# Performance work log

Hardware: AMD Instinct MI355X
Metric: run time of the kernel (lower is better)

Reference implementation:

```python
import jax, jax.numpy as jnp
import numpy as np

B, S, E = 2, 2048, 2048
H, HKV = 16, 4
G = H // HKV
QLR, KVLR = 1024, 512
DN, DR, DV = 128, 64, 128
DQK = DN + DR
EPS = 1.1920929e-07  # torch.finfo(float32).eps, F.rms_norm default


def rms_norm(x):
    return x * jax.lax.rsqrt(jnp.mean(x * x, axis=-1, keepdims=True) + EPS)


def apply_rope(x, cos, sin):
    # x: [B, S, h, D]; pairs are adjacent elements (torch view_as_complex convention)
    x0, x1 = x[..., 0::2], x[..., 1::2]            # [B,S,h,D/2]
    c = cos[None, :, None, :]
    s = sin[None, :, None, :]
    r0 = x0 * c - x1 * s
    r1 = x0 * s + x1 * c
    return jnp.stack([r0, r1], axis=-1).reshape(x.shape)


def setup_inputs() -> dict:
    key = jax.random.key(0)
    ks = jax.random.split(key, 8)
    inv_freq = 1.0 / (10000.0 ** (np.arange(0, DR, 2, dtype=np.float32) / DR))  # [DR/2]
    ang = np.arange(S, dtype=np.float32)[:, None] * inv_freq[None, :]           # [S, DR/2]
    return {
        "x": jax.random.normal(ks[0], (B, S, E), jnp.float32),
        "freqs_cos": jnp.asarray(np.cos(ang), jnp.float32),
        "freqs_sin": jnp.asarray(np.sin(ang), jnp.float32),
        "Wqa": jax.random.normal(ks[1], (QLR, E), jnp.float32) * (E ** -0.5),
        "Wqb": jax.random.normal(ks[2], (H * DQK, QLR), jnp.float32) * (QLR ** -0.5),
        "Wkva": jax.random.normal(ks[3], (KVLR + DR, E), jnp.float32) * (E ** -0.5),
        "Wkvb": jax.random.normal(ks[4], (HKV * (DN + DV), KVLR), jnp.float32) * (KVLR ** -0.5),
        "Wo": jax.random.normal(ks[5], (E, H * DV), jnp.float32) * ((H * DV) ** -0.5),
    }


def reference(x, freqs_cos, freqs_sin, Wqa, Wqb, Wkva, Wkvb, Wo):
    # Q path: low-rank down-proj -> rmsnorm -> up-proj
    q = rms_norm(x @ Wqa.T) @ Wqb.T                       # [B,S,H*DQK]
    q = q.reshape(B, S, H, DQK)
    q_nope, q_rope = q[..., :DN], q[..., DN:]
    q_rope = apply_rope(q_rope, freqs_cos, freqs_sin)
    q = jnp.concatenate([q_nope, q_rope], axis=-1)        # [B,S,H,DQK]

    # KV path: joint down-proj, shared rope key, up-proj of latent
    kv_a = x @ Wkva.T                                     # [B,S,KVLR+DR]
    kv_latent, k_rope = kv_a[..., :KVLR], kv_a[..., KVLR:]
    k_rope = jnp.broadcast_to(k_rope[:, :, None, :], (B, S, HKV, DR))
    k_rope = apply_rope(k_rope, freqs_cos, freqs_sin)     # [B,S,HKV,DR]
    kv = (rms_norm(kv_latent) @ Wkvb.T).reshape(B, S, HKV, DN + DV)
    k_nope, v = kv[..., :DN], kv[..., DN:]
    k = jnp.concatenate([k_nope, k_rope], axis=-1)        # [B,S,HKV,DQK]

    # GQA causal SDPA: group G query heads per kv head
    qg = q.reshape(B, S, HKV, G, DQK)
    scores = jnp.einsum("bsngd,btnd->bngst", qg, k) * (DQK ** -0.5)  # [B,HKV,G,S,S]
    causal = jnp.tril(jnp.ones((S, S), bool))
    scores = jnp.where(causal, scores, jnp.finfo(scores.dtype).min)
    attn = jax.nn.softmax(scores, axis=-1)
    o = jnp.einsum("bngst,btnd->bsngd", attn, v).reshape(B, S, H * DV)
    return o @ Wo.T                                        # [B,S,E]
```

## Files before the change

kernel.cpp:

```cpp
#include <hip/hip_runtime.h>
#include <cstdint>
#include <cstddef>

typedef __attribute__((ext_vector_type(4))) float f32x4;
typedef __attribute__((ext_vector_type(2))) float f32x2;
typedef __attribute__((ext_vector_type(8))) short short8;
typedef __attribute__((ext_vector_type(8))) __bf16 bf16x8;
typedef unsigned short u16;
typedef unsigned int u32;
typedef __attribute__((ext_vector_type(2))) unsigned int u32x2;
typedef __attribute__((ext_vector_type(4))) unsigned short u16x4;
typedef __attribute__((ext_vector_type(2))) unsigned short u16x2;

#define EPS_RMS 1.1920929e-07f

__device__ __forceinline__ u16 f2bf(float f) {
  union { float f; unsigned u; } v; v.f = f;
  unsigned r = v.u + 0x7FFFu + ((v.u >> 16) & 1u);
  return (u16)(r >> 16);
}
__device__ __forceinline__ float b2f(u16 x) {
  union { unsigned u; float f; } v; v.u = ((unsigned)x) << 16;
  return v.f;
}
__device__ __forceinline__ u32 cvt_pk_bf16(float lo, float hi) {
  u32 r;
  asm("v_cvt_pk_bf16_f32 %0, %1, %2" : "=v"(r) : "v"(lo), "v"(hi));
  return r;
}

template <typename V>
__device__ __forceinline__ auto mfma_try(V a, V b, f32x4 c, int)
    -> decltype(__builtin_amdgcn_mfma_f32_16x16x32_bf16(a, b, c, 0, 0, 0)) {
  return __builtin_amdgcn_mfma_f32_16x16x32_bf16(a, b, c, 0, 0, 0);
}
template <typename V>
__device__ __forceinline__ f32x4 mfma_try(V a, V b, f32x4 c, long) {
  return __builtin_amdgcn_mfma_f32_16x16x32_bf16(
      __builtin_bit_cast(bf16x8, a), __builtin_bit_cast(bf16x8, b), c, 0, 0, 0);
}
__device__ __forceinline__ f32x4 mfma_bf16(short8 a, short8 b, f32x4 c) {
  return mfma_try(a, b, c, 0);
}

__device__ __forceinline__ void load_lds16(u16* lds, const u16* g) {
  auto* gp = reinterpret_cast<const __attribute__((address_space(1))) unsigned int*>(
      reinterpret_cast<uintptr_t>(g));
  auto* lp = reinterpret_cast<__attribute__((address_space(3))) unsigned int*>(
      reinterpret_cast<uintptr_t>(lds));
  __builtin_amdgcn_global_load_lds(gp, lp, 16, 0, 0);
}

__device__ __forceinline__ float fast_exp2(float x) {
  return __builtin_amdgcn_exp2f(x);
}

template <int CTRL>
__device__ __forceinline__ float dpp_step(float v) {
  int t = __builtin_amdgcn_update_dpp(0, __builtin_bit_cast(int, v), CTRL, 0xF, 0xF, true);
  return __builtin_bit_cast(float, t);
}

__global__ __launch_bounds__(256) void cvt_bf16(const float* __restrict__ in,
                                                u16* __restrict__ out, int n4) {
  int i = blockIdx.x * 256 + threadIdx.x;
  if (i >= n4) return;
  f32x4 v = ((const f32x4*)in)[i];
  u16x4 o = {f2bf(v.x), f2bf(v.y), f2bf(v.z), f2bf(v.w)};
  ((u16x4*)out)[i] = o;
}

__global__ __launch_bounds__(256) void build_wacat(const float* __restrict__ Wqa,
                                                   const float* __restrict__ Wkva,
                                                   u16* __restrict__ out) {
  int i = blockIdx.x * 256 + threadIdx.x;
  if (i >= 851968) return;
  int r = i >> 9;
  int c4 = i & 511;
  f32x4 v = {0.f, 0.f, 0.f, 0.f};
  if (r < 1024) v = ((const f32x4*)Wqa)[r * 512 + c4];
  else if (r < 1600) v = ((const f32x4*)Wkva)[(r - 1024) * 512 + c4];
  u16x4 o = {f2bf(v.x), f2bf(v.y), f2bf(v.z), f2bf(v.w)};
  ((u16x4*)out)[i] = o;
}

template <typename OutT, int EPI>
__global__ __launch_bounds__(256) void gemm_bt(const u16* __restrict__ A,
                                               const u16* __restrict__ B,
                                               OutT* __restrict__ C,
                                               int M, int N, int K, int gx,
                                               const float* __restrict__ fc,
                                               const float* __restrict__ fs,
                                               u16* __restrict__ aux) {
  __shared__ __align__(16) u16 As[2][128 * 64];
  __shared__ __align__(16) u16 Bs[2][128 * 64];
  const int nwg = gridDim.x;
  const int cpx = nwg >> 3;
  const int swz = (blockIdx.x & 7) * cpx + (blockIdx.x >> 3);
  const int by = swz / gx, bxx = swz - by * gx;
  const int tid = threadIdx.x;
  const int lane = tid & 63, w = tid >> 6;
  const int wr = w >> 1, wc = w & 1;
  const int l16 = lane & 15, lg = lane >> 4;
  const int row0 = by * 128, col0 = bxx * 128;

  const u16* Ab = A + (size_t)row0 * K;
  const u16* Bb = B + (size_t)col0 * K;

  f32x4 acc[4][4] = {};

  int soff[4], ldst[4];
#pragma unroll
  for (int j = 0; j < 4; ++j) {
    int c = j * 256 + tid;
    int row = c >> 3;
    int rb = (c & 7) << 4;
    int sb = rb ^ ((row & 7) << 4);
    soff[j] = row * K + (sb >> 1);
    ldst[j] = c * 8;
  }

#pragma unroll
  for (int j = 0; j < 4; ++j) load_lds16(As[0] + ldst[j], Ab + soff[j]);
#pragma unroll
  for (int j = 0; j < 4; ++j) load_lds16(Bs[0] + ldst[j], Bb + soff[j]);
  __syncthreads();

  int cur = 0;
  for (int k0 = 0; k0 < K; k0 += 64) {
    if (k0 + 64 < K) {
#pragma unroll
      for (int j = 0; j < 4; ++j) load_lds16(As[cur ^ 1] + ldst[j], Ab + soff[j] + k0 + 64);
#pragma unroll
      for (int j = 0; j < 4; ++j) load_lds16(Bs[cur ^ 1] + ldst[j], Bb + soff[j] + k0 + 64);
    }
    const u16* Ac = As[cur];
    const u16* Bc = Bs[cur];
    short8 a[2][4], bfr[2][4];
#pragma unroll
    for (int mt = 0; mt < 4; ++mt) {
      const int rowA = wr * 64 + mt * 16 + l16;
      const int sw = (rowA & 7) << 4;
#pragma unroll
      for (int kk = 0; kk < 2; ++kk)
        a[kk][mt] = *(const short8*)(Ac + rowA * 64 + (((kk * 64 + lg * 16) ^ sw) >> 1));
    }
#pragma unroll
    for (int nt = 0; nt < 4; ++nt) {
      const int rowB = wc * 64 + nt * 16 + l16;
      const int sw = (rowB & 7) << 4;
#pragma unroll
      for (int kk = 0; kk < 2; ++kk)
        bfr[kk][nt] = *(const short8*)(Bc + rowB * 64 + (((kk * 64 + lg * 16) ^ sw) >> 1));
    }
#pragma unroll
    for (int kk = 0; kk < 2; ++kk)
#pragma unroll
      for (int mt = 0; mt < 4; ++mt)
#pragma unroll
        for (int nt = 0; nt < 4; ++nt)
          acc[mt][nt] = mfma_bf16(a[kk][mt], bfr[kk][nt], acc[mt][nt]);
    __syncthreads();
    cur ^= 1;
  }

  if constexpr (EPI == 0 || EPI == 1) {
#pragma unroll
    for (int mt = 0; mt < 4; ++mt)
#pragma unroll
      for (int nt = 0; nt < 4; ++nt)
#pragma unroll
        for (int i = 0; i < 4; ++i) {
          int row = row0 + wr * 64 + mt * 16 + lg * 4 + i;
          int col = col0 + wc * 64 + nt * 16 + l16;
          if constexpr (EPI == 0)
            C[(size_t)row * N + col] = acc[mt][nt][i];
          else
            C[(size_t)row * N + col] = f2bf(acc[mt][nt][i]);
        }
  } else if constexpr (EPI == 2) {
    const float qscale = 0.07216878364870322f * 1.4426950408889634f;
#pragma unroll
    for (int mt = 0; mt < 4; ++mt)
#pragma unroll
      for (int nt = 0; nt < 4; ++nt) {
        int col = col0 + wc * 64 + nt * 16 + l16;
        int hh = ((col >> 6) * 43) >> 7;
        int cin = col - hh * 192;
        int m = (cin - 128) >> 1;
#pragma unroll
        for (int i = 0; i < 4; ++i) {
          int row = row0 + wr * 64 + mt * 16 + lg * 4 + i;
          int bb = row >> 11, ss = row & 2047;
          float v = acc[mt][nt][i];
          float pv = dpp_step<0xB1>(v);
          float val = v;
          if (cin >= 128) {
            float c = fc[ss * 32 + m], sn = fs[ss * 32 + m];
            val = ((l16 & 1) == 0) ? (v * c - pv * sn) : (pv * sn + v * c);
          }
          ((u16*)C)[((size_t)((bb * 16 + hh) * 2048 + ss)) * 192 + cin] = f2bf(val * qscale);
        }
      }
  } else {
#pragma unroll
    for (int mt = 0; mt < 4; ++mt)
#pragma unroll
      for (int nt = 0; nt < 4; ++nt) {
        int col = col0 + wc * 64 + nt * 16 + l16;
        int nn = col >> 8, cin = col & 255;
        int rowb = row0 + wr * 64 + mt * 16 + lg * 4;
        int bb = rowb >> 11, ss0 = rowb & 2047;
        if (cin < 128) {
#pragma unroll
          for (int i = 0; i < 4; ++i)
            ((u16*)C)[((size_t)((bb * 4 + nn) * 2048 + ss0 + i)) * 192 + cin] =
                f2bf(acc[mt][nt][i]);
        } else {
          int dv = cin - 128;
          u16x4 o = {f2bf(acc[mt][nt][0]), f2bf(acc[mt][nt][1]),
                     f2bf(acc[mt][nt][2]), f2bf(acc[mt][nt][3])};
          *(u16x4*)(aux + ((size_t)((bb * 4 + nn) * 128 + dv)) * 2048 + ss0) = o;
        }
      }
  }
}

__global__ __launch_bounds__(256) void rms_fused(const u16* __restrict__ c1b,
                                                 const float* __restrict__ fc,
                                                 const float* __restrict__ fs,
                                                 u16* __restrict__ qlat,
                                                 u16* __restrict__ kvlat,
                                                 u16* __restrict__ Ka) {
  __shared__ float smq[4], smk[4];
  int t = blockIdx.x;
  const u16* row = c1b + (size_t)t * 1664;
  u16x4 v4u = ((const u16x4*)row)[threadIdx.x];
  u16x2 v2u = ((const u16x2*)(row + 1024))[threadIdx.x];
  float v4x = b2f(v4u.x), v4y = b2f(v4u.y), v4z = b2f(v4u.z), v4w = b2f(v4u.w);
  float v2x = b2f(v2u.x), v2y = b2f(v2u.y);
  float sq = v4x * v4x + v4y * v4y + v4z * v4z + v4w * v4w;
  float sk = v2x * v2x + v2y * v2y;
#pragma unroll
  for (int off = 32; off; off >>= 1) { sq += __shfl_xor(sq, off); sk += __shfl_xor(sk, off); }
  if ((threadIdx.x & 63) == 0) { smq[threadIdx.x >> 6] = sq; smk[threadIdx.x >> 6] = sk; }
  __syncthreads();
  float rq = rsqrtf((smq[0] + smq[1] + smq[2] + smq[3]) * (1.0f / 1024.0f) + EPS_RMS);
  float rk = rsqrtf((smk[0] + smk[1] + smk[2] + smk[3]) * (1.0f / 512.0f) + EPS_RMS);
  u16x4 oq = {f2bf(v4x * rq), f2bf(v4y * rq), f2bf(v4z * rq), f2bf(v4w * rq)};
  ((u16x4*)(qlat + (size_t)t * 1024))[threadIdx.x] = oq;
  u16x2 ok = {f2bf(v2x * rk), f2bf(v2y * rk)};
  ((u16x2*)(kvlat + (size_t)t * 512))[threadIdx.x] = ok;
  if (threadIdx.x < 32) {
    int bb = t >> 11, s = t & 2047;
    int m = threadIdx.x;
    float x0 = b2f(row[1536 + 2 * m]), x1 = b2f(row[1537 + 2 * m]);
    float c = fc[s * 32 + m], sn = fs[s * 32 + m];
    u16 r0 = f2bf(x0 * c - x1 * sn);
    u16 r1 = f2bf(x0 * sn + x1 * c);
#pragma unroll
    for (int nn = 0; nn < 4; ++nn) {
      size_t base = ((size_t)((bb * 4 + nn) * 2048 + s)) * 192 + 128;
      Ka[base + 2 * m] = r0;
      Ka[base + 2 * m + 1] = r1;
    }
  }
}

__global__ __launch_bounds__(256, 2) void attn_kernel(const u16* __restrict__ Qa,
                                                      const u16* __restrict__ Ka,
                                                      const u16* __restrict__ VTp,
                                                      u16* __restrict__ Ob) {
  __shared__ __align__(16) u16 Ks[64 * 192];
  __shared__ __align__(16) u16 Vs[128 * 64];
  __shared__ __align__(16) u32 Ppk[4][32][36];
  const int gid = blockIdx.x;
  const int bx = (gid < 256) ? (15 - (gid >> 5)) : ((gid - 256) >> 5);
  const int hb = gid & 31;
  const int b = hb >> 4;
  const int h = hb & 15;
  const int n = h >> 2;
  const int tid = threadIdx.x;
  const int lane = tid & 63;
  const int w = tid >> 6;
  const int l16 = lane & 15;
  const int lg = lane >> 4;

  const u16* Qp = Qa + ((size_t)((b * 16 + h) * 2048 + bx * 128 + w * 32)) * 192;
  const u16* Kp = Ka + ((size_t)((b * 4 + n) * 2048)) * 192;
  const u16* Vp = VTp + ((size_t)((b * 4 + n) * 128)) * 2048;

  int oK[6];
#pragma unroll
  for (int j = 0; j < 6; ++j) {
    int c = j * 256 + tid;
    int row = (c * 2731) >> 16;
    int rb = (c - row * 24) << 4;
    int sb = rb ^ ((row & 7) << 4);
    oK[j] = row * 192 + (sb >> 1);
  }
  int oV[4];
#pragma unroll
  for (int j = 0; j < 4; ++j) {
    int c = j * 256 + tid;
    int row = c >> 3;
    int rb = (c & 7) << 4;
    int sb = rb ^ ((row & 7) << 4);
    oV[j] = row * 2048 + (sb >> 1);
  }

  short8 qf[2][6];
#pragma unroll
  for (int g = 0; g < 2; ++g)
#pragma unroll
    for (int kc = 0; kc < 6; ++kc)
      qf[g][kc] = *(const short8*)(Qp + (size_t)(g * 16 + l16) * 192 + kc * 32 + lg * 8);

  float mrow[2], lrow[2];
  f32x4 oacc[2][8];
#pragma unroll
  for (int g = 0; g < 2; ++g) { mrow[g] = -1e30f; lrow[g] = 0.f; }
#pragma unroll
  for (int g = 0; g < 2; ++g)
#pragma unroll
    for (int vb = 0; vb < 8; ++vb) oacc[g][vb] = (f32x4){0.f, 0.f, 0.f, 0.f};

  const int wrow = bx * 128 + w * 32;
  const int NT = 2 * bx + 2;

  f32x4 kreg[6], vreg[4];
#pragma unroll
  for (int j = 0; j < 6; ++j) kreg[j] = *(const f32x4*)(Kp + oK[j]);
#pragma unroll
  for (int j = 0; j < 4; ++j) vreg[j] = *(const f32x4*)(Vp + oV[j]);

  for (int kt = 0; kt < NT; ++kt) {
    const int kb = kt * 64;
    __syncthreads();
#pragma unroll
    for (int j = 0; j < 6; ++j) *(f32x4*)(Ks + (j * 256 + tid) * 8) = kreg[j];
#pragma unroll
    for (int j = 0; j < 4; ++j) *(f32x4*)(Vs + (j * 256 + tid) * 8) = vreg[j];
    __syncthreads();
    if (kt + 1 < NT) {
      const int kb2 = kb + 64;
#pragma unroll
      for (int j = 0; j < 6; ++j)
        kreg[j] = *(const f32x4*)(Kp + oK[j] + (size_t)kb2 * 192);
#pragma unroll
      for (int j = 0; j < 4; ++j)
        vreg[j] = *(const f32x4*)(Vp + oV[j] + kb2);
    }
    if (kb > wrow + 31) continue;

    f32x4 sc[2][4];
#pragma unroll
    for (int g = 0; g < 2; ++g)
#pragma unroll
      for (int kn = 0; kn < 4; ++kn) sc[g][kn] = (f32x4){0.f, 0.f, 0.f, 0.f};
    __builtin_amdgcn_s_setprio(1);
#pragma unroll
    for (int kn = 0; kn < 4; ++kn) {
      const int rk = kn * 16 + l16;
      const u16* kbase = Ks + rk * 192;
      const int sw = (rk & 7) << 4;
#pragma unroll
      for (int kc = 0; kc < 6; ++kc) {
        short8 kf = *(const short8*)(kbase + (((kc * 64 + lg * 16) ^ sw) >> 1));
        sc[0][kn] = mfma_bf16(kf, qf[0][kc], sc[0][kn]);
        sc[1][kn] = mfma_bf16(kf, qf[1][kc], sc[1][kn]);
      }
    }
    __builtin_amdgcn_s_setprio(0);
    if (kb + 63 > wrow) {
#pragma unroll
      for (int g = 0; g < 2; ++g) {
        const int qabs = wrow + g * 16 + l16;
#pragma unroll
        for (int kn = 0; kn < 4; ++kn)
#pragma unroll
          for (int i = 0; i < 4; ++i)
            if (kb + kn * 16 + lg * 4 + i > qabs) sc[g][kn][i] = -1e30f;
      }
    }
    float pmax[2];
    int need = 0;
#pragma unroll
    for (int g = 0; g < 2; ++g) {
      float v = -1e30f;
#pragma unroll
      for (int kn = 0; kn < 4; ++kn)
        v = fmaxf(v, fmaxf(fmaxf(sc[g][kn][0], sc[g][kn][1]),
                           fmaxf(sc[g][kn][2], sc[g][kn][3])));
      v = fmaxf(v, __shfl_xor(v, 16));
      v = fmaxf(v, __shfl_xor(v, 32));
      pmax[g] = v;
      need |= (v > mrow[g] + 8.0f) ? 1 : 0;
    }
    if (__any(need)) {
#pragma unroll
      for (int g = 0; g < 2; ++g) {
        float mn = fmaxf(mrow[g], pmax[g]);
        float al = fast_exp2(mrow[g] - mn);
        mrow[g] = mn;
        lrow[g] *= al;
#pragma unroll
        for (int i = 0; i < 4; ++i) {
          float alq = __shfl(al, lg * 4 + i);
#pragma unroll
          for (int vb = 0; vb < 8; ++vb) oacc[g][vb][i] *= alq;
        }
      }
    }
#pragma unroll
    for (int g = 0; g < 2; ++g) {
      float rs = 0.f;
#pragma unroll
      for (int kn = 0; kn < 4; ++kn)
#pragma unroll
        for (int i = 0; i < 4; ++i) {
          float p = fast_exp2(sc[g][kn][i] - mrow[g]);
          sc[g][kn][i] = p;
          rs += p;
        }
      rs += __shfl_xor(rs, 16);
      rs += __shfl_xor(rs, 32);
      lrow[g] += rs;
    }
#pragma unroll
    for (int g = 0; g < 2; ++g) {
      const int r = g * 16 + l16;
#pragma unroll
      for (int kn = 0; kn < 4; ++kn) {
        u32x2 pk = {cvt_pk_bf16(sc[g][kn][0], sc[g][kn][1]),
                    cvt_pk_bf16(sc[g][kn][2], sc[g][kn][3])};
        *(u32x2*)&Ppk[w][r][kn * 8 + 2 * lg] = pk;
      }
    }
    short8 pa[2][2];
#pragma unroll
    for (int g = 0; g < 2; ++g) {
      const int r = g * 16 + l16;
      pa[g][0] = *(const short8*)&Ppk[w][r][lg * 4];
      pa[g][1] = *(const short8*)&Ppk[w][r][16 + lg * 4];
    }
    __builtin_amdgcn_s_setprio(1);
#pragma unroll
    for (int vb = 0; vb < 8; ++vb) {
      const int rv = vb * 16 + l16;
      const u16* vbase = Vs + rv * 64;
      const int swv = (rv & 7) << 4;
      short8 v0 = *(const short8*)(vbase + (((lg * 16) ^ swv) >> 1));
      short8 v1 = *(const short8*)(vbase + (((64 + lg * 16) ^ swv) >> 1));
      oacc[0][vb] = mfma_bf16(pa[0][0], v0, oacc[0][vb]);
      oacc[1][vb] = mfma_bf16(pa[1][0], v0, oacc[1][vb]);
      oacc[0][vb] = mfma_bf16(pa[0][1], v1, oacc[0][vb]);
      oacc[1][vb] = mfma_bf16(pa[1][1], v1, oacc[1][vb]);
    }
    __builtin_amdgcn_s_setprio(0);
  }
#pragma unroll
  for (int g = 0; g < 2; ++g) {
    float inv = 1.0f / lrow[g];
#pragma unroll
    for (int i = 0; i < 4; ++i) {
      float invq = __shfl(inv, lg * 4 + i);
      int srow = wrow + g * 16 + lg * 4 + i;
      size_t base = ((size_t)(b * 2048 + srow)) * 2048 + h * 128;
#pragma unroll
      for (int vb = 0; vb < 8; ++vb)
        Ob[base + vb * 16 + l16] = f2bf(oacc[g][vb][i] * invq);
    }
  }
}

extern "C" void kernel_launch(void* const* d_in, const int* in_sizes, int n_in,
                              void* d_out, int out_size, void* d_ws, size_t ws_size,
                              hipStream_t stream) {
  const float* x = (const float*)d_in[0];
  const float* fc = (const float*)d_in[1];
  const float* fs = (const float*)d_in[2];
  const float* Wqa = (const float*)d_in[3];
  const float* Wqb = (const float*)d_in[4];
  const float* Wkva = (const float*)d_in[5];
  const float* Wkvb = (const float*)d_in[6];
  const float* Wo = (const float*)d_in[7];
  float* out = (float*)d_out;

  char* ws = (char*)d_ws;
  u16* xb    = (u16*)(ws + 0);
  u16* wacat = (u16*)(ws + 16777216);
  u16* wqb   = (u16*)(ws + 23592960);
  u16* wkvb  = (u16*)(ws + 29884416);
  u16* wo    = (u16*)(ws + 30932992);
  u16* c1b   = (u16*)(ws + 39321600);
  u16* qlat  = (u16*)(ws + 52953088);
  u16* kvlat = (u16*)(ws + 61341696);
  u16* obf   = (u16*)(ws + 65536000);
  u16* qattn = (u16*)(ws + 82313216);
  u16* kattn = (u16*)(ws + 107479040);
  u16* vt    = (u16*)(ws + 113770496);
  if (ws_size < 117964800u) return;

  cvt_bf16<<<8192, 256, 0, stream>>>(x, xb, 2097152);
  build_wacat<<<3328, 256, 0, stream>>>(Wqa, Wkva, wacat);
  cvt_bf16<<<3072, 256, 0, stream>>>(Wqb, wqb, 786432);
  cvt_bf16<<<512, 256, 0, stream>>>(Wkvb, wkvb, 131072);
  cvt_bf16<<<4096, 256, 0, stream>>>(Wo, wo, 1048576);

  gemm_bt<u16, 1><<<416, 256, 0, stream>>>(xb, wacat, c1b, 4096, 1664, 2048, 13,
                                           nullptr, nullptr, nullptr);
  rms_fused<<<4096, 256, 0, stream>>>(c1b, fc, fs, qlat, kvlat, kattn);
  gemm_bt<u16, 2><<<768, 256, 0, stream>>>(qlat, wqb, qattn, 4096, 3072, 1024, 24,
                                           fc, fs, nullptr);
  gemm_bt<u16, 3><<<256, 256, 0, stream>>>(kvlat, wkvb, kattn, 4096, 1024, 512, 8,
                                           nullptr, nullptr, vt);
  attn_kernel<<<512, 256, 0, stream>>>(qattn, kattn, vt, obf);
  gemm_bt<float, 0><<<512, 256, 0, stream>>>(obf, wo, out, 4096, 2048, 2048, 16,
                                             nullptr, nullptr, nullptr);
}
```

Measured before the change: 244.7 us.

## Widen GEMM tiles to 128x256 with 8 waves and deeper LDS prefetch pipeline

Replaces the 128x128, 4-wave GEMM with a 128x256 tile using 512 threads (2x4 waves). It prefetches two K-tiles ahead, splits each K-step into two MFMA phases, and uses explicit waitcnt, sched and s_barrier control plus setprio around the MFMA bursts, aiming to hide global-to-LDS latency and improve reuse of the A tile. The concatenated weight is padded to 1792 rows so that N divides the wider tile, which adds some wasted compute. The workspace is also re-laid out with qattn aliasing xb. The larger LDS footprint and fewer blocks may lower occupancy or leave CUs idle on small GEMMs.

```diff
diff --git a/kernel.cpp b/kernel.cpp
--- a/kernel.cpp
+++ b/kernel.cpp
@@ -74,7 +74,7 @@
                                                    const float* __restrict__ Wkva,
                                                    u16* __restrict__ out) {
   int i = blockIdx.x * 256 + threadIdx.x;
-  if (i >= 851968) return;
+  if (i >= 917504) return;
   int r = i >> 9;
   int c4 = i & 511;
   f32x4 v = {0.f, 0.f, 0.f, 0.f};
@@ -85,82 +85,124 @@
 }
 
 template <typename OutT, int EPI>
-__global__ __launch_bounds__(256) void gemm_bt(const u16* __restrict__ A,
-                                               const u16* __restrict__ B,
-                                               OutT* __restrict__ C,
-                                               int M, int N, int K, int gx,
-                                               const float* __restrict__ fc,
-                                               const float* __restrict__ fs,
-                                               u16* __restrict__ aux) {
+__global__ __launch_bounds__(512, 2) void gemm_bt2(const u16* __restrict__ A,
+                                                   const u16* __restrict__ B,
+                                                   OutT* __restrict__ C,
+                                                   int M, int N, int K, int gx,
+                                                   const float* __restrict__ fc,
+                                                   const float* __restrict__ fs,
+                                                   u16* __restrict__ aux) {
   __shared__ __align__(16) u16 As[2][128 * 64];
-  __shared__ __align__(16) u16 Bs[2][128 * 64];
+  __shared__ __align__(16) u16 Bs[2][256 * 64];
   const int nwg = gridDim.x;
   const int cpx = nwg >> 3;
   const int swz = (blockIdx.x & 7) * cpx + (blockIdx.x >> 3);
   const int by = swz / gx, bxx = swz - by * gx;
   const int tid = threadIdx.x;
   const int lane = tid & 63, w = tid >> 6;
-  const int wr = w >> 1, wc = w & 1;
+  const int wr = w >> 2, wc = w & 3;
   const int l16 = lane & 15, lg = lane >> 4;
-  const int row0 = by * 128, col0 = bxx * 128;
+  const int row0 = by * 128, col0 = bxx * 256;
 
   const u16* Ab = A + (size_t)row0 * K;
   const u16* Bb = B + (size_t)col0 * K;
 
   f32x4 acc[4][4] = {};
 
-  int soff[4], ldst[4];
+  int soffA[2], ldA[2], soffB[4], ldB[4];
+#pragma unroll
+  for (int j = 0; j < 2; ++j) {
+    int c = j * 512 + tid;
+    int row = c >> 3;
+    int sb = ((c & 7) << 4) ^ ((row & 7) << 4);
+    soffA[j] = row * K + (sb >> 1);
+    ldA[j] = c * 8;
+  }
 #pragma unroll
   for (int j = 0; j < 4; ++j) {
-    int c = j * 256 + tid;
+    int c = j * 512 + tid;
     int row = c >> 3;
-    int rb = (c & 7) << 4;
-    int sb = rb ^ ((row & 7) << 4);
-    soff[j] = row * K + (sb >> 1);
-    ldst[j] = c * 8;
-  }
-
-#pragma unroll
-  for (int j = 0; j < 4; ++j) load_lds16(As[0] + ldst[j], Ab + soff[j]);
-#pragma unroll
-  for (int j = 0; j < 4; ++j) load_lds16(Bs[0] + ldst[j], Bb + soff[j]);
-  __syncthreads();
+    int sb = ((c & 7) << 4) ^ ((row & 7) << 4);
+    soffB[j] = row * K + (sb >> 1);
+    ldB[j] = c * 8;
+  }
+
+  const int nT = K >> 6;
+
+#pragma unroll
+  for (int j = 0; j < 2; ++j) load_lds16(As[0] + ldA[j], Ab + soffA[j]);
+#pragma unroll
+  for (int j = 0; j < 4; ++j) load_lds16(Bs[0] + ldB[j], Bb + soffB[j]);
+#pragma unroll
+  for (int j = 0; j < 2; ++j) load_lds16(As[1] + ldA[j], Ab + soffA[j] + 64);
+#pragma unroll
+  for (int j = 0; j < 4; ++j) load_lds16(Bs[1] + ldB[j], Bb + soffB[j] + 64);
+  asm volatile("s_waitcnt vmcnt(6)" ::: "memory");
+  __builtin_amdgcn_sched_barrier(0);
+  __builtin_amdgcn_s_barrier();
 
   int cur = 0;
-  for (int k0 = 0; k0 < K; k0 += 64) {
-    if (k0 + 64 < K) {
-#pragma unroll
-      for (int j = 0; j < 4; ++j) load_lds16(As[cur ^ 1] + ldst[j], Ab + soff[j] + k0 + 64);
-#pragma unroll
-      for (int j = 0; j < 4; ++j) load_lds16(Bs[cur ^ 1] + ldst[j], Bb + soff[j] + k0 + 64);
-    }
+  for (int t = 0; t < nT; ++t) {
     const u16* Ac = As[cur];
     const u16* Bc = Bs[cur];
-    short8 a[2][4], bfr[2][4];
+    short8 a0[4], b0[4];
 #pragma unroll
     for (int mt = 0; mt < 4; ++mt) {
-      const int rowA = wr * 64 + mt * 16 + l16;
-      const int sw = (rowA & 7) << 4;
-#pragma unroll
-      for (int kk = 0; kk < 2; ++kk)
-        a[kk][mt] = *(const short8*)(Ac + rowA * 64 + (((kk * 64 + lg * 16) ^ sw) >> 1));
+      int r = wr * 64 + mt * 16 + l16;
+      a0[mt] = *(const short8*)(Ac + r * 64 + (((lg * 16) ^ ((r & 7) << 4)) >> 1));
     }
 #pragma unroll
     for (int nt = 0; nt < 4; ++nt) {
-      const int rowB = wc * 64 + nt * 16 + l16;
-      const int sw = (rowB & 7) << 4;
-#pragma unroll
-      for (int kk = 0; kk < 2; ++kk)
-        bfr[kk][nt] = *(const short8*)(Bc + rowB * 64 + (((kk * 64 + lg * 16) ^ sw) >> 1));
-    }
-#pragma unroll
-    for (int kk = 0; kk < 2; ++kk)
-#pragma unroll
-      for (int mt = 0; mt < 4; ++mt)
-#pragma unroll
-        for (int nt = 0; nt < 4; ++nt)
-          acc[mt][nt] = mfma_bf16(a[kk][mt], bfr[kk][nt], acc[mt][nt]);
-    __syncthreads();
+      int r = wc * 64 + nt * 16 + l16;
+      b0[nt] = *(const short8*)(Bc + r * 64 + (((lg * 16) ^ ((r & 7) << 4)) >> 1));
+    }
+    __builtin_amdgcn_s_barrier();
+    asm volatile("s_waitcnt lgkmcnt(0)" ::: "memory");
+    __builtin_amdgcn_sched_barrier(0);
+    __builtin_amdgcn_s_setprio(1);
+#pragma unroll
+    for (int mt = 0; mt < 4; ++mt)
+#pragma unroll
+      for (int nt = 0; nt < 4; ++nt)
+        acc[mt][nt] = mfma_bf16(a0[mt], b0[nt], acc[mt][nt]);
+    __builtin_amdgcn_s_setprio(0);
+    short8 a1[4], b1[4];
+#pragma unroll
+    for (int mt = 0; mt < 4; ++mt) {
+      int r = wr * 64 + mt * 16 + l16;
+      a1[mt] = *(const short8*)(Ac + r * 64 + (((64 + lg * 16) ^ ((r & 7) << 4)) >> 1));
+    }
+#pragma unroll
+    for (int nt = 0; nt < 4; ++nt) {
+      int r = wc * 64 + nt * 16 + l16;
+      b1[nt] = *(const short8*)(Bc + r * 64 + (((64 + lg * 16) ^ ((r & 7) << 4)) >> 1));
+    }
+    asm volatile("s_waitcnt lgkmcnt(0)" ::: "memory");
+    __builtin_amdgcn_sched_barrier(0);
+    __builtin_amdgcn_s_barrier();
+    if (t + 2 < nT) {
+      const int ko = (t + 2) << 6;
+#pragma unroll
+      for (int j = 0; j < 2; ++j) load_lds16(As[cur] + ldA[j], Ab + soffA[j] + ko);
+#pragma unroll
+      for (int j = 0; j < 4; ++j) load_lds16(Bs[cur] + ldB[j], Bb + soffB[j] + ko);
+    }
+    __builtin_amdgcn_s_setprio(1);
+#pragma unroll
+    for (int mt = 0; mt < 4; ++mt)
+#pragma unroll
+      for (int nt = 0; nt < 4; ++nt)
+        acc[mt][nt] = mfma_bf16(a1[mt], b1[nt], acc[mt][nt]);
+    __builtin_amdgcn_s_setprio(0);
+    if (t + 1 < nT) {
+      if (t + 2 < nT) {
+        asm volatile("s_waitcnt vmcnt(6)" ::: "memory");
+      } else {
+        asm volatile("s_waitcnt vmcnt(0)" ::: "memory");
+      }
+      __builtin_amdgcn_sched_barrier(0);
+      __builtin_amdgcn_s_barrier();
+    }
     cur ^= 1;
   }
 
@@ -234,7 +276,7 @@
                                                  u16* __restrict__ Ka) {
   __shared__ float smq[4], smk[4];
   int t = blockIdx.x;
-  const u16* row = c1b + (size_t)t * 1664;
+  const u16* row = c1b + (size_t)t * 1792;
   u16x4 v4u = ((const u16x4*)row)[threadIdx.x];
   u16x2 v2u = ((const u16x2*)(row + 1024))[threadIdx.x];
   float v4x = b2f(v4u.x), v4y = b2f(v4u.y), v4z = b2f(v4u.z), v4w = b2f(v4u.w);
@@ -490,32 +532,32 @@
   char* ws = (char*)d_ws;
   u16* xb    = (u16*)(ws + 0);
   u16* wacat = (u16*)(ws + 16777216);
-  u16* wqb   = (u16*)(ws + 23592960);
-  u16* wkvb  = (u16*)(ws + 29884416);
-  u16* wo    = (u16*)(ws + 30932992);
-  u16* c1b   = (u16*)(ws + 39321600);
-  u16* qlat  = (u16*)(ws + 52953088);
-  u16* kvlat = (u16*)(ws + 61341696);
-  u16* obf   = (u16*)(ws + 65536000);
-  u16* qattn = (u16*)(ws + 82313216);
-  u16* kattn = (u16*)(ws + 107479040);
-  u16* vt    = (u16*)(ws + 113770496);
-  if (ws_size < 117964800u) return;
+  u16* qattn = (u16*)(ws + 0);
+  u16* wqb   = (u16*)(ws + 25165824);
+  u16* wkvb  = (u16*)(ws + 31457280);
+  u16* wo    = (u16*)(ws + 32505856);
+  u16* c1b   = (u16*)(ws + 40894464);
+  u16* qlat  = (u16*)(ws + 55574528);
+  u16* kvlat = (u16*)(ws + 63963136);
+  u16* obf   = (u16*)(ws + 68157440);
+  u16* kattn = (u16*)(ws + 84934656);
+  u16* vt    = (u16*)(ws + 91226112);
+  if (ws_size < 95420416u) return;
 
   cvt_bf16<<<8192, 256, 0, stream>>>(x, xb, 2097152);
-  build_wacat<<<3328, 256, 0, stream>>>(Wqa, Wkva, wacat);
+  build_wacat<<<3584, 256, 0, stream>>>(Wqa, Wkva, wacat);
   cvt_bf16<<<3072, 256, 0, stream>>>(Wqb, wqb, 786432);
   cvt_bf16<<<512, 256, 0, stream>>>(Wkvb, wkvb, 131072);
   cvt_bf16<<<4096, 256, 0, stream>>>(Wo, wo, 1048576);
 
-  gemm_bt<u16, 1><<<416, 256, 0, stream>>>(xb, wacat, c1b, 4096, 1664, 2048, 13,
-                                           nullptr, nullptr, nullptr);
+  gemm_bt2<u16, 1><<<224, 512, 0, stream>>>(xb, wacat, c1b, 4096, 1792, 2048, 7,
+                                            nullptr, nullptr, nullptr);
   rms_fused<<<4096, 256, 0, stream>>>(c1b, fc, fs, qlat, kvlat, kattn);
-  gemm_bt<u16, 2><<<768, 256, 0, stream>>>(qlat, wqb, qattn, 4096, 3072, 1024, 24,
-                                           fc, fs, nullptr);
-  gemm_bt<u16, 3><<<256, 256, 0, stream>>>(kvlat, wkvb, kattn, 4096, 1024, 512, 8,
-                                           nullptr, nullptr, vt);
+  gemm_bt2<u16, 2><<<384, 512, 0, stream>>>(qlat, wqb, qattn, 4096, 3072, 1024, 12,
+                                            fc, fs, nullptr);
+  gemm_bt2<u16, 3><<<128, 512, 0, stream>>>(kvlat, wkvb, kattn, 4096, 1024, 512, 4,
+                                            nullptr, nullptr, vt);
   attn_kernel<<<512, 256, 0, stream>>>(qattn, kattn, vt, obf);
-  gemm_bt<float, 0><<<512, 256, 0, stream>>>(obf, wo, out, 4096, 2048, 2048, 16,
-                                             nullptr, nullptr, nullptr);
-}
+  gemm_bt2<float, 0><<<256, 512, 0, stream>>>(obf, wo, out, 4096, 2048, 2048, 8,
+                                              nullptr, nullptr, nullptr);
+}
```

Result: slower. 253.5 us (+3.6%).

## Shrink attention blocks to 64 query rows and read V directly from global

Applied to the files above, without the earlier changes.

The attention kernel now uses 128-thread blocks, each covering 64 query rows, and launches twice as many blocks. The block-to-tile map uses a serpentine order across bands to balance causal work. V tiles are no longer staged in shared memory; each wave loads V fragments straight from global memory before the PV MFMAs. This cuts LDS use and barrier traffic and raises occupancy, at the cost of redundant global V loads per wave and less K reuse per block.

```diff
diff --git a/kernel.cpp b/kernel.cpp
--- a/kernel.cpp
+++ b/kernel.cpp
@@ -267,18 +267,20 @@
   }
 }
 
-__global__ __launch_bounds__(256, 2) void attn_kernel(const u16* __restrict__ Qa,
+__global__ __launch_bounds__(128, 2) void attn_kernel(const u16* __restrict__ Qa,
                                                       const u16* __restrict__ Ka,
                                                       const u16* __restrict__ VTp,
                                                       u16* __restrict__ Ob) {
   __shared__ __align__(16) u16 Ks[64 * 192];
-  __shared__ __align__(16) u16 Vs[128 * 64];
-  __shared__ __align__(16) u32 Ppk[4][32][36];
+  __shared__ __align__(16) u32 Ppk[2][32][36];
   const int gid = blockIdx.x;
-  const int bx = (gid < 256) ? (15 - (gid >> 5)) : ((gid - 256) >> 5);
-  const int hb = gid & 31;
-  const int b = hb >> 4;
-  const int h = hb & 15;
+  const int band = gid >> 8, idx = gid & 255;
+  const int pos = (band & 1) ? (255 - idx) : idx;
+  const int rank = band * 256 + pos;
+  const int qx = 31 - (rank >> 5);
+  const int bh = rank & 31;
+  const int b = bh >> 4;
+  const int h = bh & 15;
   const int n = h >> 2;
   const int tid = threadIdx.x;
   const int lane = tid & 63;
@@ -286,28 +288,19 @@
   const int l16 = lane & 15;
   const int lg = lane >> 4;
 
-  const u16* Qp = Qa + ((size_t)((b * 16 + h) * 2048 + bx * 128 + w * 32)) * 192;
+  const u16* Qp = Qa + ((size_t)((b * 16 + h) * 2048 + qx * 64 + w * 32)) * 192;
   const u16* Kp = Ka + ((size_t)((b * 4 + n) * 2048)) * 192;
   const u16* Vp = VTp + ((size_t)((b * 4 + n) * 128)) * 2048;
 
-  int oK[6];
-#pragma unroll
-  for (int j = 0; j < 6; ++j) {
-    int c = j * 256 + tid;
+  int oK[12];
+#pragma unroll
+  for (int j = 0; j < 12; ++j) {
+    int c = j * 128 + tid;
     int row = (c * 2731) >> 16;
     int rb = (c - row * 24) << 4;
     int sb = rb ^ ((row & 7) << 4);
     oK[j] = row * 192 + (sb >> 1);
   }
-  int oV[4];
-#pragma unroll
-  for (int j = 0; j < 4; ++j) {
-    int c = j * 256 + tid;
-    int row = c >> 3;
-    int rb = (c & 7) << 4;
-    int sb = rb ^ ((row & 7) << 4);
-    oV[j] = row * 2048 + (sb >> 1);
-  }
 
   short8 qf[2][6];
 #pragma unroll
@@ -325,33 +318,25 @@
 #pragma unroll
     for (int vb = 0; vb < 8; ++vb) oacc[g][vb] = (f32x4){0.f, 0.f, 0.f, 0.f};
 
-  const int wrow = bx * 128 + w * 32;
-  const int NT = 2 * bx + 2;
-
-  f32x4 kreg[6], vreg[4];
-#pragma unroll
-  for (int j = 0; j < 6; ++j) kreg[j] = *(const f32x4*)(Kp + oK[j]);
-#pragma unroll
-  for (int j = 0; j < 4; ++j) vreg[j] = *(const f32x4*)(Vp + oV[j]);
+  const int wrow = qx * 64 + w * 32;
+  const int NT = qx + 1;
+
+  f32x4 kreg[12];
+#pragma unroll
+  for (int j = 0; j < 12; ++j) kreg[j] = *(const f32x4*)(Kp + oK[j]);
 
   for (int kt = 0; kt < NT; ++kt) {
     const int kb = kt * 64;
     __syncthreads();
 #pragma unroll
-    for (int j = 0; j < 6; ++j) *(f32x4*)(Ks + (j * 256 + tid) * 8) = kreg[j];
-#pragma unroll
-    for (int j = 0; j < 4; ++j) *(f32x4*)(Vs + (j * 256 + tid) * 8) = vreg[j];
+    for (int j = 0; j < 12; ++j) *(f32x4*)(Ks + (j * 128 + tid) * 8) = kreg[j];
     __syncthreads();
     if (kt + 1 < NT) {
       const int kb2 = kb + 64;
 #pragma unroll
-      for (int j = 0; j < 6; ++j)
+      for (int j = 0; j < 12; ++j)
         kreg[j] = *(const f32x4*)(Kp + oK[j] + (size_t)kb2 * 192);
-#pragma unroll
-      for (int j = 0; j < 4; ++j)
-        vreg[j] = *(const f32x4*)(Vp + oV[j] + kb2);
-    }
-    if (kb > wrow + 31) continue;
+    }
 
     f32x4 sc[2][4];
 #pragma unroll
@@ -446,16 +431,23 @@
     }
     __builtin_amdgcn_s_setprio(1);
 #pragma unroll
-    for (int vb = 0; vb < 8; ++vb) {
-      const int rv = vb * 16 + l16;
-      const u16* vbase = Vs + rv * 64;
-      const int swv = (rv & 7) << 4;
-      short8 v0 = *(const short8*)(vbase + (((lg * 16) ^ swv) >> 1));
-      short8 v1 = *(const short8*)(vbase + (((64 + lg * 16) ^ swv) >> 1));
-      oacc[0][vb] = mfma_bf16(pa[0][0], v0, oacc[0][vb]);
-      oacc[1][vb] = mfma_bf16(pa[1][0], v0, oacc[1][vb]);
-      oacc[0][vb] = mfma_bf16(pa[0][1], v1, oacc[0][vb]);
-      oacc[1][vb] = mfma_bf16(pa[1][1], v1, oacc[1][vb]);
+    for (int hf = 0; hf < 2; ++hf) {
+      short8 vv[4][2];
+#pragma unroll
+      for (int q = 0; q < 4; ++q) {
+        const int vb = hf * 4 + q;
+        const u16* vrow = Vp + (size_t)(vb * 16 + l16) * 2048 + kb;
+        vv[q][0] = *(const short8*)(vrow + lg * 8);
+        vv[q][1] = *(const short8*)(vrow + 32 + lg * 8);
+      }
+#pragma unroll
+      for (int q = 0; q < 4; ++q) {
+        const int vb = hf * 4 + q;
+        oacc[0][vb] = mfma_bf16(pa[0][0], vv[q][0], oacc[0][vb]);
+        oacc[1][vb] = mfma_bf16(pa[1][0], vv[q][0], oacc[1][vb]);
+        oacc[0][vb] = mfma_bf16(pa[0][1], vv[q][1], oacc[0][vb]);
+        oacc[1][vb] = mfma_bf16(pa[1][1], vv[q][1], oacc[1][vb]);
+      }
     }
     __builtin_amdgcn_s_setprio(0);
   }
@@ -515,7 +507,7 @@
                                            fc, fs, nullptr);
   gemm_bt<u16, 3><<<256, 256, 0, stream>>>(kvlat, wkvb, kattn, 4096, 1024, 512, 8,
                                            nullptr, nullptr, vt);
-  attn_kernel<<<512, 256, 0, stream>>>(qattn, kattn, vt, obf);
+  attn_kernel<<<1024, 128, 0, stream>>>(qattn, kattn, vt, obf);
   gemm_bt<float, 0><<<512, 256, 0, stream>>>(obf, wo, out, 4096, 2048, 2048, 16,
                                              nullptr, nullptr, nullptr);
 }
```

After: 364.5 us. 1.49x slower.

## Split KV range for long causal query blocks and merge partials in a combine kernel

Applied to the files above, without the earlier changes.

Query blocks 8–15, whose causal KV range is longest, are now each processed by two workgroups that cover half the KV tiles. Each half writes a normalized bf16 partial output plus its row max and row sum into reused workspace. A new combine kernel merges the two halves with log-sum-exp weights. The goal is to shorten the critical path set by the largest causal blocks and balance work across CUs, at the cost of an extra launch, extra partial traffic and one more bf16 rounding of the output.

```diff
diff --git a/kernel.cpp b/kernel.cpp
--- a/kernel.cpp
+++ b/kernel.cpp
@@ -270,23 +270,48 @@
 __global__ __launch_bounds__(256, 2) void attn_kernel(const u16* __restrict__ Qa,
                                                       const u16* __restrict__ Ka,
                                                       const u16* __restrict__ VTp,
-                                                      u16* __restrict__ Ob) {
+                                                      u16* __restrict__ Ob,
+                                                      u16* __restrict__ pO,
+                                                      float* __restrict__ pML) {
   __shared__ __align__(16) u16 Ks[64 * 192];
   __shared__ __align__(16) u16 Vs[128 * 64];
   __shared__ __align__(16) u32 Ppk[4][32][36];
-  const int gid = blockIdx.x;
-  const int bx = (gid < 256) ? (15 - (gid >> 5)) : ((gid - 256) >> 5);
-  const int hb = gid & 31;
-  const int b = hb >> 4;
-  const int h = hb & 15;
+  int bxv, half, split, o;
+  {
+    const int gid = blockIdx.x;
+    if      (gid < 64)  { split = 1; bxv = 15; o = gid; }
+    else if (gid < 96)  { split = 0; bxv = 7;  o = gid - 64; }
+    else if (gid < 160) { split = 1; bxv = 14; o = gid - 96; }
+    else if (gid < 224) { split = 1; bxv = 13; o = gid - 160; }
+    else if (gid < 256) { split = 0; bxv = 6;  o = gid - 224; }
+    else if (gid < 320) { split = 1; bxv = 12; o = gid - 256; }
+    else if (gid < 384) { split = 1; bxv = 11; o = gid - 320; }
+    else if (gid < 416) { split = 0; bxv = 5;  o = gid - 384; }
+    else if (gid < 480) { split = 1; bxv = 10; o = gid - 416; }
+    else if (gid < 544) { split = 1; bxv = 9;  o = gid - 480; }
+    else if (gid < 576) { split = 0; bxv = 4;  o = gid - 544; }
+    else if (gid < 640) { split = 1; bxv = 8;  o = gid - 576; }
+    else if (gid < 672) { split = 0; bxv = 3;  o = gid - 640; }
+    else if (gid < 704) { split = 0; bxv = 2;  o = gid - 672; }
+    else if (gid < 736) { split = 0; bxv = 1;  o = gid - 704; }
+    else                { split = 0; bxv = 0;  o = gid - 736; }
+  }
+  half = split ? (o >> 5) : 0;
+  const int bhv = o & 31;
+  const int b = bhv >> 4;
+  const int h = bhv & 15;
   const int n = h >> 2;
+  const int NTfull = 2 * bxv + 2;
+  const int k0t = (split && half) ? (bxv + 1) : 0;
+  const int k1t = (split && !half) ? (bxv + 1) : NTfull;
+
   const int tid = threadIdx.x;
   const int lane = tid & 63;
   const int w = tid >> 6;
   const int l16 = lane & 15;
   const int lg = lane >> 4;
 
-  const u16* Qp = Qa + ((size_t)((b * 16 + h) * 2048 + bx * 128 + w * 32)) * 192;
+  const u16* Qp = Qa + ((size_t)((b * 16 + h) * 2048 + bxv * 128 + w * 32)) * 192;
   const u16* Kp = Ka + ((size_t)((b * 4 + n) * 2048)) * 192;
   const u16* Vp = VTp + ((size_t)((b * 4 + n) * 128)) * 2048;
 
@@ -325,16 +350,15 @@
 #pragma unroll
     for (int vb = 0; vb < 8; ++vb) oacc[g][vb] = (f32x4){0.f, 0.f, 0.f, 0.f};
 
-  const int wrow = bx * 128 + w * 32;
-  const int NT = 2 * bx + 2;
+  const int wrow = bxv * 128 + w * 32;
 
   f32x4 kreg[6], vreg[4];
 #pragma unroll
-  for (int j = 0; j < 6; ++j) kreg[j] = *(const f32x4*)(Kp + oK[j]);
-#pragma unroll
-  for (int j = 0; j < 4; ++j) vreg[j] = *(const f32x4*)(Vp + oV[j]);
-
-  for (int kt = 0; kt < NT; ++kt) {
+  for (int j = 0; j < 6; ++j) kreg[j] = *(const f32x4*)(Kp + oK[j] + (size_t)(k0t * 64) * 192);
+#pragma unroll
+  for (int j = 0; j < 4; ++j) vreg[j] = *(const f32x4*)(Vp + oV[j] + k0t * 64);
+
+  for (int kt = k0t; kt < k1t; ++kt) {
     const int kb = kt * 64;
     __syncthreads();
 #pragma unroll
@@ -342,7 +366,7 @@
 #pragma unroll
     for (int j = 0; j < 4; ++j) *(f32x4*)(Vs + (j * 256 + tid) * 8) = vreg[j];
     __syncthreads();
-    if (kt + 1 < NT) {
+    if (kt + 1 < k1t) {
       const int kb2 = kb + 64;
 #pragma unroll
       for (int j = 0; j < 6; ++j)
@@ -459,18 +483,74 @@
     }
     __builtin_amdgcn_s_setprio(0);
   }
-#pragma unroll
-  for (int g = 0; g < 2; ++g) {
-    float inv = 1.0f / lrow[g];
-#pragma unroll
-    for (int i = 0; i < 4; ++i) {
-      float invq = __shfl(inv, lg * 4 + i);
-      int srow = wrow + g * 16 + lg * 4 + i;
-      size_t base = ((size_t)(b * 2048 + srow)) * 2048 + h * 128;
-#pragma unroll
-      for (int vb = 0; vb < 8; ++vb)
-        Ob[base + vb * 16 + l16] = f2bf(oacc[g][vb][i] * invq);
-    }
+
+  if (!split) {
+#pragma unroll
+    for (int g = 0; g < 2; ++g) {
+      float inv = 1.0f / lrow[g];
+#pragma unroll
+      for (int i = 0; i < 4; ++i) {
+        float invq = __shfl(inv, lg * 4 + i);
+        int srow = wrow + g * 16 + lg * 4 + i;
+        size_t base = ((size_t)(b * 2048 + srow)) * 2048 + h * 128;
+#pragma unroll
+        for (int vb = 0; vb < 8; ++vb)
+          Ob[base + vb * 16 + l16] = f2bf(oacc[g][vb][i] * invq);
+      }
+    }
+  } else {
+    const int p = ((bxv - 8) * 32 + bhv) * 2 + half;
+    u16* po = pO + (size_t)p * 16384;
+    float* pml = pML + p * 256;
+#pragma unroll
+    for (int g = 0; g < 2; ++g) {
+      float inv = 1.0f / lrow[g];
+#pragma unroll
+      for (int i = 0; i < 4; ++i) {
+        float invq = __shfl(inv, lg * 4 + i);
+        int lr = w * 32 + g * 16 + lg * 4 + i;
+#pragma unroll
+        for (int vb = 0; vb < 8; ++vb)
+          po[lr * 128 + vb * 16 + l16] = f2bf(oacc[g][vb][i] * invq);
+      }
+      if (lg == 0) {
+        int lr0 = w * 32 + g * 16 + l16;
+        pml[lr0] = mrow[g];
+        pml[128 + lr0] = lrow[g];
+      }
+    }
+  }
+}
+
+__global__ __launch_bounds__(256) void attn_combine(const u16* __restrict__ pO,
+                                                    const float* __restrict__ pML,
+                                                    u16* __restrict__ Ob) {
+  const int grp = blockIdx.x;
+  const int bxv = 8 + (grp >> 5);
+  const int bhv = grp & 31;
+  const int b = bhv >> 4, h = bhv & 15;
+  const int r = threadIdx.x >> 1;
+  const int ch = threadIdx.x & 1;
+  const int p1 = ((bxv - 8) * 32 + bhv) * 2, p2 = p1 + 1;
+  float m1 = pML[p1 * 256 + r], l1 = pML[p1 * 256 + 128 + r];
+  float m2 = pML[p2 * 256 + r], l2 = pML[p2 * 256 + 128 + r];
+  float m = fmaxf(m1, m2);
+  float a1 = fast_exp2(m1 - m) * l1;
+  float a2 = fast_exp2(m2 - m) * l2;
+  float inv = 1.0f / (a1 + a2);
+  float w1 = a1 * inv, w2 = a2 * inv;
+  const short8* o1 = (const short8*)(pO + (size_t)p1 * 16384 + r * 128 + ch * 64);
+  const short8* o2 = (const short8*)(pO + (size_t)p2 * 16384 + r * 128 + ch * 64);
+  short8* ob = (short8*)(Ob + ((size_t)(b * 2048 + bxv * 128 + r)) * 2048 + h * 128 + ch * 64);
+#pragma unroll
+  for (int j = 0; j < 8; ++j) {
+    short8 v1 = o1[j];
+    short8 v2 = o2[j];
+    short8 ov;
+#pragma unroll
+    for (int e = 0; e < 8; ++e)
+      ov[e] = (short)f2bf(b2f((u16)v1[e]) * w1 + b2f((u16)v2[e]) * w2);
+    ob[j] = ov;
   }
 }
 
@@ -500,6 +580,8 @@
   u16* qattn = (u16*)(ws + 82313216);
   u16* kattn = (u16*)(ws + 107479040);
   u16* vt    = (u16*)(ws + 113770496);
+  u16* pO    = (u16*)(ws + 0);
+  float* pML = (float*)(ws + 16777216);
   if (ws_size < 117964800u) return;
 
   cvt_bf16<<<8192, 256, 0, stream>>>(x, xb, 2097152);
@@ -515,7 +597,8 @@
                                            fc, fs, nullptr);
   gemm_bt<u16, 3><<<256, 256, 0, stream>>>(kvlat, wkvb, kattn, 4096, 1024, 512, 8,
                                            nullptr, nullptr, vt);
-  attn_kernel<<<512, 256, 0, stream>>>(qattn, kattn, vt, obf);
+  attn_kernel<<<768, 256, 0, stream>>>(qattn, kattn, vt, obf, pO, pML);
+  attn_combine<<<256, 256, 0, stream>>>(pO, pML, obf);
   gemm_bt<float, 0><<<512, 256, 0, stream>>>(obf, wo, out, 4096, 2048, 2048, 16,
                                              nullptr, nullptr, nullptr);
 }
```

New measurement: 258.2 us. 5.5% more time.
